# Performance work log

Measured on AMD Instinct MI355X. Metric: run time of the kernel, lower is better.

## Reference

```python
import jax, jax.numpy as jnp
import numpy as np

NPOINT = 1024
RADIUS = 0.2
NSAMPLE = 32


def furthest_point_sampling(xyz, npoint):
    # xyz: (B, N, 3) -> (B, npoint) int32 indices
    B, N, _ = xyz.shape

    def step(carry, _):
        dist, far = carry
        centroid = jnp.take_along_axis(xyz, far[:, None, None], axis=1)  # (B,1,3)
        d = jnp.sum((xyz - centroid) ** 2, axis=-1)                       # (B,N)
        dist = jnp.minimum(dist, d)
        new_far = jnp.argmax(dist, axis=-1).astype(jnp.int32)
        return (dist, new_far), far

    init = (jnp.full((B, N), 1e10, xyz.dtype), jnp.zeros((B,), jnp.int32))
    _, idx = jax.lax.scan(step, init, None, length=npoint)
    return idx.T  # (B, npoint)


def ball_query(xyz, new_xyz, radius, nsample):
    # xyz: (B,N,3), new_xyz: (B,S,3) -> (B,S,nsample) int32 indices
    N = xyz.shape[1]
    d2 = jnp.sum((new_xyz[:, :, None, :] - xyz[:, None, :, :]) ** 2, axis=-1)  # (B,S,N)
    # pick first `nsample` indices within radius (CUDA ball_query semantics)
    key = jnp.where(d2 < radius * radius, jnp.arange(N, dtype=jnp.int32)[None, None, :], N)
    idx = jnp.sort(key, axis=-1)[..., :nsample]          # (B,S,nsample)
    first = idx[..., :1]
    idx = jnp.where(idx == N, first, idx)                # pad with first valid
    return jnp.clip(idx, 0, N - 1).astype(jnp.int32)     # guard empty balls


def sa_forward(xyz, features, W1, s1, b1, W2, s2, b2, W3, s3, b3):
    B, N, _ = xyz.shape
    center_idx = furthest_point_sampling(xyz, NPOINT)                     # (B,S)
    new_xyz = jnp.take_along_axis(xyz, center_idx[..., None], axis=1)     # (B,S,3)

    idx = ball_query(xyz, new_xyz, RADIUS, NSAMPLE)                       # (B,S,K)
    # group xyz (relative coords) and features
    g_xyz = jnp.take_along_axis(xyz[:, None], idx[..., None], axis=2)     # (B,S,K,3)
    g_xyz = g_xyz - new_xyz[:, :, None, :]
    feats_n = jnp.swapaxes(features, 1, 2)                                # (B,N,C)
    g_feat = jnp.take_along_axis(feats_n[:, None], idx[..., None], axis=2)  # (B,S,K,C)
    g = jnp.concatenate([g_xyz, g_feat], axis=-1)                         # (B,S,K,3+C)
    x = jnp.transpose(g, (0, 3, 1, 2))                                    # (B,3+C,S,K)

    # 1x1 conv MLP with (folded) BN affine + ReLU
    for W, s, b in ((W1, s1, b1), (W2, s2, b2), (W3, s3, b3)):
        x = jax.nn.relu(jnp.einsum('oi,bisk->bosk', W, x)
                        * s[None, :, None, None] + b[None, :, None, None])
    new_features = jnp.max(x, axis=-1)                                    # (B,Cout,S)
    return new_xyz, new_features


def setup_inputs() -> dict:
    key = jax.random.key(0)
    ks = jax.random.split(key, 11)
    B, N, C = 4, 16384, 64
    return {
        'xyz': jax.random.uniform(ks[0], (B, N, 3), jnp.float32),
        'features': jax.random.normal(ks[1], (B, C, N), jnp.float32),
        'W1': jax.random.normal(ks[2], (64, C + 3), jnp.float32) * 0.1,
        's1': jax.random.uniform(ks[3], (64,), jnp.float32),
        'b1': jax.random.normal(ks[4], (64,), jnp.float32) * 0.1,
        'W2': jax.random.normal(ks[5], (64, 64), jnp.float32) * 0.1,
        's2': jax.random.uniform(ks[6], (64,), jnp.float32),
        'b2': jax.random.normal(ks[7], (64,), jnp.float32) * 0.1,
        'W3': jax.random.normal(ks[8], (128, 64), jnp.float32) * 0.1,
        's3': jax.random.uniform(ks[9], (128,), jnp.float32),
        'b3': jax.random.normal(ks[10], (128,), jnp.float32) * 0.1,
    }


def reference(xyz, features, W1, s1, b1, W2, s2, b2, W3, s3, b3):
    return sa_forward(xyz, features, W1, s1, b1, W2, s2, b2, W3, s3, b3)
```

## Files before the change

### kernel.cpp

```cpp
#include <hip/hip_runtime.h>
#include <cstdint>
#include <cstddef>

#define BATCH   4
#define NPTS    16384
#define NPOINT  1024
#define NSAMPLE 32
#define CIN     67
#define R2f     0.04f

#define FPS_T   1024
#define FPS_P   16

#define RPT16(M) M(0)M(1)M(2)M(3)M(4)M(5)M(6)M(7)M(8)M(9)M(10)M(11)M(12)M(13)M(14)M(15)

template <int CTRL, int RMASK>
__device__ __forceinline__ void amax_dpp(float& v, int& i) {
  int nv = __builtin_amdgcn_update_dpp(__float_as_int(v), __float_as_int(v),
                                       CTRL, RMASK, 0xf, false);
  int ni = __builtin_amdgcn_update_dpp(i, i, CTRL, RMASK, 0xf, false);
  float fv = __int_as_float(nv);
  bool tk = (fv > v) || (fv == v && ni < i);
  v = tk ? fv : v;
  i = tk ? ni : i;
}

__global__ void __launch_bounds__(FPS_T)
fps_kernel(const float* __restrict__ xyz, float* __restrict__ out_newxyz)
{
  __shared__ float2 pxy[NPTS];
  __shared__ float  s_wv[2][16];
  __shared__ int    s_wi[2][16];

  const int b = blockIdx.x;
  const float* base = xyz + (size_t)b * NPTS * 3;
  const int t = threadIdx.x;
  const int lane = t & 63, w = t >> 6;

#define DECLV(i) float pz##i, dd##i;
  RPT16(DECLV)
#undef DECLV
#define LOADV(i) { const int idx = ((i) << 10) + t; \
                   const float* p = base + (size_t)idx * 3; \
                   pxy[idx] = make_float2(p[0], p[1]); \
                   pz##i = p[2]; dd##i = 1e10f; }
  RPT16(LOADV)
#undef LOADV
#define PINV(i) asm("" : "+v"(pz##i), "+v"(dd##i));
  RPT16(PINV)
#undef PINV

  float cx = base[0], cy = base[1], cz = base[2];

  for (int it = 0; it < NPOINT; ++it) {
    if (t == 0) {
      int o = (b * NPOINT + it) * 3;
      out_newxyz[o + 0] = cx;
      out_newxyz[o + 1] = cy;
      out_newxyz[o + 2] = cz;
    }
    float bv = -1.0f; int bl = 0;
#define STEPV(i) { \
    float2 q = pxy[((i) << 10) + t]; \
    float dx = __fsub_rn(q.x, cx); \
    float dy = __fsub_rn(q.y, cy); \
    float dz = __fsub_rn(pz##i, cz); \
    float d2 = __fadd_rn(__fadd_rn(__fmul_rn(dx, dx), __fmul_rn(dy, dy)), \
                         __fmul_rn(dz, dz)); \
    float nd = fminf(dd##i, d2); dd##i = nd; \
    bool tk = nd > bv;   \
    bv = tk ? nd : bv; \
    bl = tk ? (i) : bl; }
    RPT16(STEPV)
#undef STEPV
    int bi = (bl << 10) + t;

    amax_dpp<0x121, 0xf>(bv, bi);
    amax_dpp<0x122, 0xf>(bv, bi);
    amax_dpp<0x124, 0xf>(bv, bi);
    amax_dpp<0x128, 0xf>(bv, bi);
    amax_dpp<0x142, 0xa>(bv, bi);
    amax_dpp<0x143, 0xc>(bv, bi);

    const int par = it & 1;
    if (lane == 63) { s_wv[par][w] = bv; s_wi[par][w] = bi; }
    __syncthreads();

    float gv = s_wv[par][lane & 15];
    int   gi = s_wi[par][lane & 15];
    amax_dpp<0x121, 0xf>(gv, gi);
    amax_dpp<0x122, 0xf>(gv, gi);
    amax_dpp<0x124, 0xf>(gv, gi);
    amax_dpp<0x128, 0xf>(gv, gi);

    int far = __builtin_amdgcn_readfirstlane(gi);
    cx = base[far * 3 + 0];
    cy = base[far * 3 + 1];
    cz = base[far * 3 + 2];
  }
}

__global__ __launch_bounds__(256) void transpose_kernel(
    const float* __restrict__ f, float* __restrict__ ft)
{
  __shared__ float tile[64][65];
  int b  = blockIdx.x >> 8;
  int n0 = (blockIdx.x & 255) << 6;
  for (int v = threadIdx.x; v < 64 * 64; v += 256) {
    int c = v >> 6, j = v & 63;
    tile[c][j] = f[((size_t)(b * 64 + c)) * NPTS + n0 + j];
  }
  __syncthreads();
  for (int v = threadIdx.x; v < 64 * 64; v += 256) {
    int j = v >> 6, c = v & 63;
    ft[((size_t)(b * NPTS + n0 + j)) * 64 + c] = tile[c][j];
  }
}

__global__ __launch_bounds__(1024) void mlp_kernel(
    const float* __restrict__ xyz,
    const float* __restrict__ feats,
    const float* __restrict__ featsT,
    const float* __restrict__ nx,
    const float* __restrict__ W1, const float* __restrict__ s1, const float* __restrict__ b1,
    const float* __restrict__ W2, const float* __restrict__ s2, const float* __restrict__ b2,
    const float* __restrict__ W3, const float* __restrict__ s3, const float* __restrict__ b3,
    float* __restrict__ outF)
{
  __shared__ float W1t[CIN * 64];
  __shared__ float W2t[64 * 64];
  __shared__ float sb[512];
  __shared__ float xs[CIN * 34];
  __shared__ float h1[64 * 34];
  __shared__ float h2[64 * 34];
  __shared__ int   hm[128];
  __shared__ int   lid8[8][NSAMPLE];

  const int tid = threadIdx.x;
  const int lane = tid & 63, w = tid >> 6;

  for (int v = tid; v < CIN * 64; v += 1024) {
    int o = v / CIN, i = v - o * CIN;
    W1t[i * 64 + o] = W1[v];
  }
  for (int v = tid; v < 64 * 64; v += 1024) {
    int o = v >> 6, i = v & 63;
    W2t[i * 64 + o] = W2[v];
  }
  if (tid < 64)       sb[tid]       = s1[tid];
  else if (tid < 128) sb[tid]       = b1[tid - 64];
  else if (tid < 192) sb[tid]       = s2[tid - 128];
  else if (tid < 256) sb[tid]       = b2[tid - 192];
  else if (tid < 384) sb[tid]       = s3[tid - 256];
  else if (tid < 512) sb[tid]       = b3[tid - 384];

  if (w < 8) {
    int g = (blockIdx.x << 3) + w;
    int b = g >> 10;
    const float* base = xyz + (size_t)b * NPTS * 3;
    float cx = nx[g * 3 + 0], cy = nx[g * 3 + 1], cz = nx[g * 3 + 2];
    int cnt = 0, fidx = -1;
    for (int c0 = 0; c0 < NPTS && cnt < NSAMPLE; c0 += 64) {
      int i = c0 + lane;
      float dx = __fsub_rn(base[i * 3 + 0], cx);
      float dy = __fsub_rn(base[i * 3 + 1], cy);
      float dz = __fsub_rn(base[i * 3 + 2], cz);
      float d2 = __fadd_rn(__fadd_rn(__fmul_rn(dx, dx), __fmul_rn(dy, dy)),
                           __fmul_rn(dz, dz));
      bool pred = d2 < R2f;
      unsigned long long mk = __ballot(pred);
      if (pred) {
        int rank = cnt + __popcll(mk & ((1ull << lane) - 1ull));
        if (rank < NSAMPLE) lid8[w][rank] = i;
        if (rank == 0) fidx = i;
      }
      cnt += __popcll(mk);
    }
#pragma unroll
    for (int off = 32; off >= 1; off >>= 1) {
      int o = __shfl_xor(fidx, off);
      fidx = o > fidx ? o : fidx;
    }
    if (lane >= cnt && lane < NSAMPLE) lid8[w][lane] = fidx;
  }
  __syncthreads();

  for (int ci = 0; ci < 8; ++ci) {
    int g = (blockIdx.x << 3) + ci;
    int b = g >> 10, m = g & 1023;

    {
      int k = tid >> 5, c0 = tid & 31;
      int id = lid8[ci][k];
      for (int c = c0; c < CIN; c += 32) {
        float val;
        if (c < 3)
          val = __fsub_rn(xyz[((size_t)b * NPTS + id) * 3 + c], nx[g * 3 + c]);
        else if (featsT)
          val = featsT[((size_t)b * NPTS + id) * 64 + (c - 3)];
        else
          val = feats[((size_t)(b * 64 + (c - 3))) * NPTS + id];
        xs[c * 34 + k] = val;
      }
      if (tid < 128) hm[tid] = 0;
    }
    __syncthreads();

    {
      int oc = tid & 63, k0 = (tid >> 6) << 1;
      float a0 = 0.f, a1 = 0.f;
#pragma unroll 4
      for (int i = 0; i < CIN; ++i) {
        float ww = W1t[i * 64 + oc];
        a0 = fmaf(ww, xs[i * 34 + k0], a0);
        a1 = fmaf(ww, xs[i * 34 + k0 + 1], a1);
      }
      float s = sb[oc], bb = sb[64 + oc];
      h1[oc * 34 + k0]     = fmaxf(fmaf(a0, s, bb), 0.f);
      h1[oc * 34 + k0 + 1] = fmaxf(fmaf(a1, s, bb), 0.f);
    }
    __syncthreads();

    {
      int oc = tid & 63, k0 = (tid >> 6) << 1;
      float a0 = 0.f, a1 = 0.f;
#pragma unroll 4
      for (int i = 0; i < 64; ++i) {
        float ww = W2t[i * 64 + oc];
        a0 = fmaf(ww, h1[i * 34 + k0], a0);
        a1 = fmaf(ww, h1[i * 34 + k0 + 1], a1);
      }
      float s = sb[128 + oc], bb = sb[192 + oc];
      h2[oc * 34 + k0]     = fmaxf(fmaf(a0, s, bb), 0.f);
      h2[oc * 34 + k0 + 1] = fmaxf(fmaf(a1, s, bb), 0.f);
    }
    __syncthreads();

    {
      int oc = tid & 127, k0 = (tid >> 7) << 2;
      const float4* W3v = reinterpret_cast<const float4*>(W3);
      float a0 = 0.f, a1 = 0.f, a2 = 0.f, a3 = 0.f;
#pragma unroll 4
      for (int i4 = 0; i4 < 16; ++i4) {
        float4 wv = W3v[oc * 16 + i4];
        const float* hr = &h2[(i4 * 4) * 34 + k0];
        a0 = fmaf(wv.x, hr[0], a0); a1 = fmaf(wv.x, hr[1], a1);
        a2 = fmaf(wv.x, hr[2], a2); a3 = fmaf(wv.x, hr[3], a3);
        hr += 34;
        a0 = fmaf(wv.y, hr[0], a0); a1 = fmaf(wv.y, hr[1], a1);
        a2 = fmaf(wv.y, hr[2], a2); a3 = fmaf(wv.y, hr[3], a3);
        hr += 34;
        a0 = fmaf(wv.z, hr[0], a0); a1 = fmaf(wv.z, hr[1], a1);
        a2 = fmaf(wv.z, hr[2], a2); a3 = fmaf(wv.z, hr[3], a3);
        hr += 34;
        a0 = fmaf(wv.w, hr[0], a0); a1 = fmaf(wv.w, hr[1], a1);
        a2 = fmaf(wv.w, hr[2], a2); a3 = fmaf(wv.w, hr[3], a3);
      }
      float s = sb[256 + oc], bb = sb[384 + oc];
      float v0 = fmaxf(fmaf(a0, s, bb), 0.f);
      float v1 = fmaxf(fmaf(a1, s, bb), 0.f);
      float v2 = fmaxf(fmaf(a2, s, bb), 0.f);
      float v3 = fmaxf(fmaf(a3, s, bb), 0.f);
      float mv = fmaxf(fmaxf(v0, v1), fmaxf(v2, v3));
      atomicMax(&hm[oc], __float_as_int(mv));
    }
    __syncthreads();

    if (tid < 128)
      outF[(((size_t)b * 128 + tid) << 10) + m] = __int_as_float(hm[tid]);
    __syncthreads();
  }
}

extern "C" void kernel_launch(void* const* d_in, const int* in_sizes, int n_in,
                              void* d_out, int out_size, void* d_ws, size_t ws_size,
                              hipStream_t stream)
{
  if (n_in < 11) return;
  const float* xyz   = (const float*)d_in[0];
  const float* feats = (const float*)d_in[1];
  const float* W1 = (const float*)d_in[2];
  const float* s1 = (const float*)d_in[3];
  const float* b1 = (const float*)d_in[4];
  const float* W2 = (const float*)d_in[5];
  const float* s2 = (const float*)d_in[6];
  const float* b2 = (const float*)d_in[7];
  const float* W3 = (const float*)d_in[8];
  const float* s3 = (const float*)d_in[9];
  const float* b3 = (const float*)d_in[10];
  float* out = (float*)d_out;

  float* featsT = nullptr;
  size_t needT = (size_t)BATCH * NPTS * 64 * sizeof(float);
  if (ws_size >= needT) featsT = (float*)d_ws;

  fps_kernel<<<BATCH, FPS_T, 0, stream>>>(xyz, out);
  if (featsT) transpose_kernel<<<BATCH * 256, 256, 0, stream>>>(feats, featsT);
  mlp_kernel<<<512, 1024, 0, stream>>>(xyz, feats, featsT, out,
                                       W1, s1, b1, W2, s2, b2, W3, s3, b3,
                                       out + BATCH * NPOINT * 3);
}
```

Before: 2.449 ms.

## Split furthest point sampling across multiple blocks per batch with global atomic sync

Furthest point sampling now runs on 8 workgroups per batch instead of one. Each workgroup holds 2048 points in registers and computes a local argmax, then merges it through a packed 64-bit atomic max key in global memory, with a counter-based spin barrier at each iteration. This spreads the serial 1024-iteration loop over more compute units to shorten per-iteration work. In exchange it adds a global atomic round-trip and a spin-wait on every iteration, and it relies on all 32 workgroups being co-resident.

```diff
diff --git a/kernel.cpp b/kernel.cpp
--- a/kernel.cpp
+++ b/kernel.cpp
@@ -9,9 +9,11 @@
 #define CIN     67
 #define R2f     0.04f
 
-#define FPS_T   1024
-#define FPS_P   16
-
+#define FPS_KB  8
+#define FPS_T   512
+#define FPS_P   4
+
+#define RPT4(M)  M(0)M(1)M(2)M(3)
 #define RPT16(M) M(0)M(1)M(2)M(3)M(4)M(5)M(6)M(7)M(8)M(9)M(10)M(11)M(12)M(13)M(14)M(15)
 
 template <int CTRL, int RMASK>
@@ -26,7 +28,98 @@
 }
 
 __global__ void __launch_bounds__(FPS_T)
-fps_kernel(const float* __restrict__ xyz, float* __restrict__ out_newxyz)
+fps_multi(const float* __restrict__ xyz, float* __restrict__ out_newxyz,
+          unsigned long long* __restrict__ skey,
+          unsigned int* __restrict__ scnt)
+{
+  const int b   = blockIdx.x >> 3;
+  const int blk = blockIdx.x & 7;
+  const float* base = xyz + (size_t)b * NPTS * 3;
+  const int t = threadIdx.x;
+  const int lane = t & 63, w = t >> 6;
+
+#define DECLV(i) float px##i, py##i, pz##i, dd##i;
+  RPT4(DECLV)
+#undef DECLV
+#define LOADV(i) { const float* p = base + (size_t)((blk << 11) + ((i) << 9) + t) * 3; \
+                   px##i = p[0]; py##i = p[1]; pz##i = p[2]; dd##i = 1e10f; }
+  RPT4(LOADV)
+#undef LOADV
+
+  __shared__ float s_wv[2][8];
+  __shared__ int   s_wi[2][8];
+  __shared__ int   s_far;
+
+  float cx = base[0], cy = base[1], cz = base[2];
+
+  for (int it = 0; it < NPOINT; ++it) {
+    if (blk == 0 && t == 0) {
+      int o = (b * NPOINT + it) * 3;
+      out_newxyz[o + 0] = cx;
+      out_newxyz[o + 1] = cy;
+      out_newxyz[o + 2] = cz;
+    }
+    float bv = -1.0f; int bl = 0;
+#define STEPV(i) { \
+    float dx = __fsub_rn(px##i, cx); \
+    float dy = __fsub_rn(py##i, cy); \
+    float dz = __fsub_rn(pz##i, cz); \
+    float d2 = __fadd_rn(__fadd_rn(__fmul_rn(dx, dx), __fmul_rn(dy, dy)), \
+                         __fmul_rn(dz, dz)); \
+    float nd = fminf(dd##i, d2); dd##i = nd; \
+    bool tk = nd > bv;   \
+    bv = tk ? nd : bv; \
+    bl = tk ? (i) : bl; }
+    RPT4(STEPV)
+#undef STEPV
+    int bi = (blk << 11) + (bl << 9) + t;
+
+    amax_dpp<0x121, 0xf>(bv, bi);
+    amax_dpp<0x122, 0xf>(bv, bi);
+    amax_dpp<0x124, 0xf>(bv, bi);
+    amax_dpp<0x128, 0xf>(bv, bi);
+    amax_dpp<0x142, 0xa>(bv, bi);
+    amax_dpp<0x143, 0xc>(bv, bi);
+
+    const int par = it & 1;
+    if (lane == 63) { s_wv[par][w] = bv; s_wi[par][w] = bi; }
+    __syncthreads();
+
+    float gv = s_wv[par][lane & 7];
+    int   gi = s_wi[par][lane & 7];
+    amax_dpp<0x121, 0xf>(gv, gi);
+    amax_dpp<0x122, 0xf>(gv, gi);
+    amax_dpp<0x124, 0xf>(gv, gi);
+
+    if (t == 0) {
+      unsigned long long key =
+          ((unsigned long long)(it + 1) << 46)
+        | ((unsigned long long)__float_as_uint(gv) << 14)
+        | (unsigned long long)(16383 - gi);
+      __hip_atomic_fetch_max(&skey[b * 2 + par], key,
+                             __ATOMIC_RELAXED, __HIP_MEMORY_SCOPE_AGENT);
+      __hip_atomic_fetch_add(&scnt[b], 1u,
+                             __ATOMIC_RELEASE, __HIP_MEMORY_SCOPE_AGENT);
+      const unsigned int target = (unsigned int)FPS_KB * (unsigned int)(it + 1);
+      while (__hip_atomic_load(&scnt[b], __ATOMIC_ACQUIRE,
+                               __HIP_MEMORY_SCOPE_AGENT) < target)
+        __builtin_amdgcn_s_sleep(1);
+      unsigned long long kk =
+          __hip_atomic_load(&skey[b * 2 + par], __ATOMIC_RELAXED,
+                            __HIP_MEMORY_SCOPE_AGENT);
+      s_far = 16383 - (int)(kk & 0x3FFFull);
+    }
+    __syncthreads();
+
+    int far = __builtin_amdgcn_readfirstlane(s_far);
+    cx = base[far * 3 + 0];
+    cy = base[far * 3 + 1];
+    cz = base[far * 3 + 2];
+  }
+}
+
+__global__ void __launch_bounds__(1024)
+fps_single(const float* __restrict__ xyz, float* __restrict__ out_newxyz)
 {
   __shared__ float2 pxy[NPTS];
   __shared__ float  s_wv[2][16];
@@ -46,9 +139,6 @@
                    pz##i = p[2]; dd##i = 1e10f; }
   RPT16(LOADV)
 #undef LOADV
-#define PINV(i) asm("" : "+v"(pz##i), "+v"(dd##i));
-  RPT16(PINV)
-#undef PINV
 
   float cx = base[0], cy = base[1], cz = base[2];
 
@@ -68,7 +158,7 @@
     float d2 = __fadd_rn(__fadd_rn(__fmul_rn(dx, dx), __fmul_rn(dy, dy)), \
                          __fmul_rn(dz, dz)); \
     float nd = fminf(dd##i, d2); dd##i = nd; \
-    bool tk = nd > bv;   \
+    bool tk = nd > bv; \
     bv = tk ? nd : bv; \
     bl = tk ? (i) : bl; }
     RPT16(STEPV)
@@ -290,11 +380,21 @@
   const float* b3 = (const float*)d_in[10];
   float* out = (float*)d_out;
 
+  const size_t SYNC_BYTES = 256;
+  size_t needT = (size_t)BATCH * NPTS * 64 * sizeof(float);
   float* featsT = nullptr;
-  size_t needT = (size_t)BATCH * NPTS * 64 * sizeof(float);
-  if (ws_size >= needT) featsT = (float*)d_ws;
-
-  fps_kernel<<<BATCH, FPS_T, 0, stream>>>(xyz, out);
+  if (ws_size >= SYNC_BYTES + needT)
+    featsT = (float*)((char*)d_ws + SYNC_BYTES);
+
+  if (ws_size >= SYNC_BYTES) {
+    hipMemsetAsync(d_ws, 0, SYNC_BYTES, stream);
+    unsigned long long* skey = (unsigned long long*)d_ws;
+    unsigned int* scnt = (unsigned int*)((char*)d_ws + 64);
+    fps_multi<<<BATCH * FPS_KB, FPS_T, 0, stream>>>(xyz, out, skey, scnt);
+  } else {
+    fps_single<<<BATCH, 1024, 0, stream>>>(xyz, out);
+  }
+
   if (featsT) transpose_kernel<<<BATCH * 256, 256, 0, stream>>>(feats, featsT);
   mlp_kernel<<<512, 1024, 0, stream>>>(xyz, feats, featsT, out,
                                        W1, s1, b1, W2, s2, b2, W3, s3, b3,
```

New measurement: 3.620 ms. 1.48x slower.
